# Optimization experiments

Measured on AMD Instinct MI355X. Metric: run time of the kernel, lower is better.

Reference implementation:

```python
import jax, jax.numpy as jnp
import numpy as np

N_NODES = 4096        # number of sum nodes in this layer
N_CHILD = 16384       # total number of child-layer nodes
DEGREE = 64           # fan-in per sum node
NNZ = N_NODES * DEGREE
BATCH = 128


def setup_inputs() -> dict:
    key = jax.random.key(0)
    k1, k2, k3 = jax.random.split(key, 3)
    child_ll = jax.random.normal(k1, (BATCH, N_CHILD), dtype=jnp.float32)
    log_w = jax.random.normal(k2, (NNZ,), dtype=jnp.float32)
    # each sum node has exactly DEGREE incoming edges (sorted segment ids)
    rows = jnp.repeat(jnp.arange(N_NODES, dtype=jnp.int32), DEGREE)
    cols = jax.random.randint(k3, (NNZ,), 0, N_CHILD, dtype=jnp.int32)
    return {"child_ll": child_ll, "log_w": log_w, "rows": rows, "cols": cols}


def _segment_logsumexp(v, seg, num_segments):
    # v: [E, ...], seg: [E] -> [num_segments, ...], numerically stable
    m = jax.ops.segment_max(v, seg, num_segments=num_segments)
    m = jax.lax.stop_gradient(m)
    s = jax.ops.segment_sum(jnp.exp(v - m[seg]), seg, num_segments=num_segments)
    return m + jnp.log(s)


def reference(child_ll, log_w, rows, cols):
    # per-edge weighted child log-likelihood: [E, B]
    v = child_ll.T[cols] + log_w[:, None]
    # unnormalized sum-node log-likelihood: [N, B]
    ll = _segment_logsumexp(v, rows, N_NODES)
    # per-node log normalization constant logsumexp(log_w) over each row: [N]
    log_z = _segment_logsumexp(log_w, rows, N_NODES)
    return (ll - log_z[:, None]).T  # [B, N]
```

## Files before the change

### kernel.cpp

```cpp
#include <hip/hip_runtime.h>
#include <hip/hip_bf16.h>

#define N_NODES 4096
#define N_CHILD 16384
#define DEGREE  64
#define BATCH   128
#define NT      8

__global__ __launch_bounds__(256)
void exp_transpose_kernel(const float* __restrict__ in,
                          __hip_bfloat16* __restrict__ out) {
    __shared__ float tile[32][33];
    const int c0 = blockIdx.x * 32;
    const int b0 = blockIdx.y * 32;
    const int tx = threadIdx.x;
    const int ty = threadIdx.y;
#pragma unroll
    for (int j = 0; j < 32; j += 8)
        tile[ty + j][tx] = __expf(in[(size_t)(b0 + ty + j) * N_CHILD + (c0 + tx)]);
    __syncthreads();
#pragma unroll
    for (int j = 0; j < 32; j += 8)
        out[(size_t)(c0 + ty + j) * BATCH + (b0 + tx)] =
            __float2bfloat16(tile[tx][ty + j]);
}

__global__ __launch_bounds__(256)
void sum_layer_kernel(const __hip_bfloat16* __restrict__ childE,
                      const float* __restrict__ log_w,
                      const int*   __restrict__ cols,
                      float* __restrict__ out)
{
    const int tid  = threadIdx.x;
    const int wave = __builtin_amdgcn_readfirstlane(tid >> 6);
    const int lane = tid & 63;
    const int n0   = blockIdx.x * NT;

    __shared__ float res[NT][130];

    const unsigned int* __restrict__ rowE = (const unsigned int*)childE;

#pragma unroll
    for (int t = 0; t < 2; ++t) {
        const int jl = wave * 2 + t;
        const int e0 = (n0 + jl) * DEGREE;

        const float ew = __expf(log_w[e0 + lane]);
        float sw = ew;
#pragma unroll
        for (int off = 32; off >= 1; off >>= 1)
            sw += __shfl_xor(sw, off);
        const float lz = __logf(sw);

        float s0a = 0.f, s0b = 0.f, s1a = 0.f, s1b = 0.f;
#pragma unroll
        for (int d = 0; d < DEGREE; d += 2) {
            const int ca = cols[e0 + d];
            const int cb = cols[e0 + d + 1];
            const float ewa = __shfl(ew, d);
            const float ewb = __shfl(ew, d + 1);
            const unsigned int ua = rowE[ca * 64 + lane];
            const unsigned int ub = rowE[cb * 64 + lane];
            s0a = fmaf(__uint_as_float(ua << 16),          ewa, s0a);
            s1a = fmaf(__uint_as_float(ua & 0xffff0000u),  ewa, s1a);
            s0b = fmaf(__uint_as_float(ub << 16),          ewb, s0b);
            s1b = fmaf(__uint_as_float(ub & 0xffff0000u),  ewb, s1b);
        }

        float2 r;
        r.x = __logf(s0a + s0b) - lz;
        r.y = __logf(s1a + s1b) - lz;
        *(float2*)&res[jl][2 * lane] = r;
    }

    __syncthreads();

#pragma unroll
    for (int p = 0; p < 4; ++p) {
        const int idx = p * 256 + tid;
        const int j = idx & (NT - 1);
        const int b = idx >> 3;
        out[(size_t)b * N_NODES + n0 + j] = res[j][b];
    }
}

extern "C" void kernel_launch(void* const* d_in, const int* in_sizes, int n_in,
                              void* d_out, int out_size, void* d_ws, size_t ws_size,
                              hipStream_t stream) {
    const float* child_ll = (const float*)d_in[0];
    const float* log_w    = (const float*)d_in[1];
    const int*   cols     = (const int*)d_in[3];
    float*       out      = (float*)d_out;

    __hip_bfloat16* childE = (__hip_bfloat16*)d_ws;

    {
        dim3 tb(32, 8), tg(N_CHILD / 32, BATCH / 32);
        exp_transpose_kernel<<<tg, tb, 0, stream>>>(child_ll, childE);
    }

    sum_layer_kernel<<<N_NODES / NT, 256, 0, stream>>>(childE, log_w, cols, out);
}
```

Measured before the change: 75.50 us.

## Fuse exp-transpose and sum-layer into one cooperative kernel with grid sync

Merges the exp/transpose pre-pass and the sum-node kernel into a single cooperative launch of 512 blocks. Each block first transposes four 32x32 tiles into the bf16 workspace, then all blocks meet at a grid-wide barrier before running the same per-node weighted-sum and log logic. This removes one kernel launch and the gap between the two kernels. In exchange it adds the cost of a grid barrier and a cooperative launch, and it caps parallelism to blocks that can all be resident at once.

```diff
diff --git a/kernel.cpp b/kernel.cpp
--- a/kernel.cpp
+++ b/kernel.cpp
@@ -1,42 +1,55 @@
 #include <hip/hip_runtime.h>
 #include <hip/hip_bf16.h>
+#include <hip/hip_cooperative_groups.h>
+
+namespace cg = cooperative_groups;
 
 #define N_NODES 4096
 #define N_CHILD 16384
 #define DEGREE  64
 #define BATCH   128
 #define NT      8
+#define NBLK    512
 
-__global__ __launch_bounds__(256)
-void exp_transpose_kernel(const float* __restrict__ in,
-                          __hip_bfloat16* __restrict__ out) {
+__global__ __launch_bounds__(256, 2)
+void fused_sum_layer(const float* __restrict__ child_ll,
+                     const float* __restrict__ log_w,
+                     const int*   __restrict__ cols,
+                     float* __restrict__ out,
+                     __hip_bfloat16* __restrict__ childE)
+{
+    const int tid = threadIdx.x;
+    const int bid = blockIdx.x;
+
     __shared__ float tile[32][33];
-    const int c0 = blockIdx.x * 32;
-    const int b0 = blockIdx.y * 32;
-    const int tx = threadIdx.x;
-    const int ty = threadIdx.y;
+    __shared__ float res[NT][130];
+
+    {
+        const int tx = tid & 31;
+        const int ty = tid >> 5;
+        for (int t = 0; t < 4; ++t) {
+            const int tile_id = bid * 4 + t;
+            const int c0 = (tile_id >> 2) * 32;
+            const int b0 = (tile_id & 3) * 32;
 #pragma unroll
-    for (int j = 0; j < 32; j += 8)
-        tile[ty + j][tx] = __expf(in[(size_t)(b0 + ty + j) * N_CHILD + (c0 + tx)]);
-    __syncthreads();
+            for (int j = 0; j < 32; j += 8)
+                tile[ty + j][tx] =
+                    __expf(child_ll[(size_t)(b0 + ty + j) * N_CHILD + (c0 + tx)]);
+            __syncthreads();
 #pragma unroll
-    for (int j = 0; j < 32; j += 8)
-        out[(size_t)(c0 + ty + j) * BATCH + (b0 + tx)] =
-            __float2bfloat16(tile[tx][ty + j]);
-}
+            for (int j = 0; j < 32; j += 8)
+                childE[(size_t)(c0 + ty + j) * BATCH + (b0 + tx)] =
+                    __float2bfloat16(tile[tx][ty + j]);
+            __syncthreads();
+        }
+    }
 
-__global__ __launch_bounds__(256)
-void sum_layer_kernel(const __hip_bfloat16* __restrict__ childE,
-                      const float* __restrict__ log_w,
-                      const int*   __restrict__ cols,
-                      float* __restrict__ out)
-{
-    const int tid  = threadIdx.x;
+    __threadfence();
+    cg::this_grid().sync();
+
     const int wave = __builtin_amdgcn_readfirstlane(tid >> 6);
     const int lane = tid & 63;
-    const int n0   = blockIdx.x * NT;
-
-    __shared__ float res[NT][130];
+    const int n0   = bid * NT;
 
     const unsigned int* __restrict__ rowE = (const unsigned int*)childE;
 
@@ -91,13 +104,10 @@
     const float* log_w    = (const float*)d_in[1];
     const int*   cols     = (const int*)d_in[3];
     float*       out      = (float*)d_out;
-
     __hip_bfloat16* childE = (__hip_bfloat16*)d_ws;
 
-    {
-        dim3 tb(32, 8), tg(N_CHILD / 32, BATCH / 32);
-        exp_transpose_kernel<<<tg, tb, 0, stream>>>(child_ll, childE);
-    }
-
-    sum_layer_kernel<<<N_NODES / NT, 256, 0, stream>>>(childE, log_w, cols, out);
+    void* args[] = {(void*)&child_ll, (void*)&log_w, (void*)&cols,
+                    (void*)&out, (void*)&childE};
+    hipLaunchCooperativeKernel((void*)fused_sum_layer, dim3(NBLK), dim3(256),
+                               args, 0, stream);
 }
```

New measurement: 197.5 us. 2.62x slower.

## Split each node's 64-edge reduction across two waves in 1024-thread blocks

Applied to the files above, without the earlier changes.

Each sum node now gets two waves, and each wave reduces 32 of the node's edges instead of one wave looping over two nodes and 64 edges each. The partial sums and weight normalizers meet in shared memory, then one pass computes the logs and writes the output. The aim is more waves in flight and shorter dependent load chains per wave, to hide gather latency. The cost is an extra shared-memory combine step and larger blocks, whose register use is capped by the launch bounds.

```diff
diff --git a/kernel.cpp b/kernel.cpp
--- a/kernel.cpp
+++ b/kernel.cpp
@@ -5,7 +5,7 @@
 #define N_CHILD 16384
 #define DEGREE  64
 #define BATCH   128
-#define NT      8
+#define NN      8
 
 __global__ __launch_bounds__(256)
 void exp_transpose_kernel(const float* __restrict__ in,
@@ -25,62 +25,58 @@
             __float2bfloat16(tile[tx][ty + j]);
 }
 
-__global__ __launch_bounds__(256)
+__global__ __launch_bounds__(1024, 8)
 void sum_layer_kernel(const __hip_bfloat16* __restrict__ childE,
                       const float* __restrict__ log_w,
                       const int*   __restrict__ cols,
                       float* __restrict__ out)
 {
     const int tid  = threadIdx.x;
-    const int wave = __builtin_amdgcn_readfirstlane(tid >> 6);
+    const int wv   = __builtin_amdgcn_readfirstlane(tid >> 6);
+    const int j    = wv >> 1;
+    const int h    = wv & 1;
     const int lane = tid & 63;
-    const int n0   = blockIdx.x * NT;
+    const int n0   = blockIdx.x * NN;
+    const int e0   = (n0 + j) * DEGREE + h * 32;
 
-    __shared__ float res[NT][130];
+    __shared__ float2 part[NN][2][65];
+    __shared__ float  swp[NN][2];
+
+    const float ew = __expf(log_w[e0 + (lane & 31)]);
+    float sw = ew;
+#pragma unroll
+    for (int off = 16; off >= 1; off >>= 1)
+        sw += __shfl_xor(sw, off);
+    if (lane == 0) swp[j][h] = sw;
 
     const unsigned int* __restrict__ rowE = (const unsigned int*)childE;
 
+    float s0a = 0.f, s0b = 0.f, s1a = 0.f, s1b = 0.f;
 #pragma unroll
-    for (int t = 0; t < 2; ++t) {
-        const int jl = wave * 2 + t;
-        const int e0 = (n0 + jl) * DEGREE;
-
-        const float ew = __expf(log_w[e0 + lane]);
-        float sw = ew;
-#pragma unroll
-        for (int off = 32; off >= 1; off >>= 1)
-            sw += __shfl_xor(sw, off);
-        const float lz = __logf(sw);
-
-        float s0a = 0.f, s0b = 0.f, s1a = 0.f, s1b = 0.f;
-#pragma unroll
-        for (int d = 0; d < DEGREE; d += 2) {
-            const int ca = cols[e0 + d];
-            const int cb = cols[e0 + d + 1];
-            const float ewa = __shfl(ew, d);
-            const float ewb = __shfl(ew, d + 1);
-            const unsigned int ua = rowE[ca * 64 + lane];
-            const unsigned int ub = rowE[cb * 64 + lane];
-            s0a = fmaf(__uint_as_float(ua << 16),          ewa, s0a);
-            s1a = fmaf(__uint_as_float(ua & 0xffff0000u),  ewa, s1a);
-            s0b = fmaf(__uint_as_float(ub << 16),          ewb, s0b);
-            s1b = fmaf(__uint_as_float(ub & 0xffff0000u),  ewb, s1b);
-        }
-
-        float2 r;
-        r.x = __logf(s0a + s0b) - lz;
-        r.y = __logf(s1a + s1b) - lz;
-        *(float2*)&res[jl][2 * lane] = r;
+    for (int d = 0; d < 32; d += 2) {
+        const int ca = cols[e0 + d];
+        const int cb = cols[e0 + d + 1];
+        const float ewa = __shfl(ew, d);
+        const float ewb = __shfl(ew, d + 1);
+        const unsigned int ua = rowE[ca * 64 + lane];
+        const unsigned int ub = rowE[cb * 64 + lane];
+        s0a = fmaf(__uint_as_float(ua << 16),          ewa, s0a);
+        s1a = fmaf(__uint_as_float(ua & 0xffff0000u),  ewa, s1a);
+        s0b = fmaf(__uint_as_float(ub << 16),          ewb, s0b);
+        s1b = fmaf(__uint_as_float(ub & 0xffff0000u),  ewb, s1b);
     }
+    part[j][h][lane] = make_float2(s0a + s0b, s1a + s1b);
 
     __syncthreads();
 
-#pragma unroll
-    for (int p = 0; p < 4; ++p) {
-        const int idx = p * 256 + tid;
-        const int j = idx & (NT - 1);
-        const int b = idx >> 3;
-        out[(size_t)b * N_NODES + n0 + j] = res[j][b];
+    {
+        const int jo = tid & (NN - 1);
+        const int b  = tid >> 3;
+        const float2 p0 = part[jo][0][b >> 1];
+        const float2 p1 = part[jo][1][b >> 1];
+        const float s = (b & 1) ? (p0.y + p1.y) : (p0.x + p1.x);
+        const float lz = __logf(swp[jo][0] + swp[jo][1]);
+        out[(size_t)b * N_NODES + n0 + jo] = __logf(s) - lz;
     }
 }
 
@@ -99,5 +95,5 @@
         exp_transpose_kernel<<<tg, tb, 0, stream>>>(child_ll, childE);
     }
 
-    sum_layer_kernel<<<N_NODES / NT, 256, 0, stream>>>(childE, log_w, cols, out);
+    sum_layer_kernel<<<N_NODES / NN, 1024, 0, stream>>>(childE, log_w, cols, out);
 }
```

Result: faster. 72.61 us (-3.8%).
